# Performance work log

Hardware: AMD Instinct MI355X
Metric: run time of the kernel (lower is better)

Reference implementation:

```python
import jax, jax.numpy as jnp
import numpy as np

N_NODES = 50000

def _gcn_conv(x, W, b, src, dst, num_nodes):
    # PyG GCNConv: linear transform, then D^{-1/2} A_hat D^{-1/2} aggregation (A_hat has self-loops).
    xw = x @ W                                   # [N, out]
    ones = jnp.ones(src.shape[0], dtype=x.dtype)
    deg = jax.ops.segment_sum(ones, dst, num_segments=num_nodes)  # in-degree incl. self loop
    dinv = jnp.where(deg > 0, jax.lax.rsqrt(deg), 0.0)
    norm = dinv[src] * dinv[dst]                 # [E]
    msg = xw[src] * norm[:, None]                # [E, out] gather + scale
    out = jax.ops.segment_sum(msg, dst, num_segments=num_nodes)   # scatter-add
    return out + b

def _add_self_loops(edge_index, num_nodes):
    loop = jnp.arange(num_nodes, dtype=edge_index.dtype)
    src = jnp.concatenate([edge_index[0], loop])
    dst = jnp.concatenate([edge_index[1], loop])
    return src, dst

def setup_inputs() -> dict:
    key = jax.random.key(0)
    k = jax.random.split(key, 6)
    in_dim, hid_dim, out_dim = 256, 128, 64
    n_edges = 800000
    x = jax.random.normal(k[0], (N_NODES, in_dim), dtype=jnp.float32)
    edge_index = jax.random.randint(k[1], (2, n_edges), 0, N_NODES, dtype=jnp.int64)
    W1 = jax.random.normal(k[2], (in_dim, hid_dim), dtype=jnp.float32) / np.sqrt(in_dim)
    b1 = jnp.zeros((hid_dim,), dtype=jnp.float32)
    W2 = jax.random.normal(k[3], (hid_dim, out_dim), dtype=jnp.float32) / np.sqrt(hid_dim)
    b2 = jnp.zeros((out_dim,), dtype=jnp.float32)
    return {"x": x, "edge_index": edge_index, "W1": W1, "b1": b1, "W2": W2, "b2": b2}

def reference(x, edge_index, W1, b1, W2, b2):
    src, dst = _add_self_loops(edge_index, N_NODES)
    h = jnp.tanh(_gcn_conv(x, W1, b1, src, dst, N_NODES))
    out = _gcn_conv(h, W2, b2, src, dst, N_NODES)
    return out
```

## Files before the change

kernel.cpp:

```cpp
#include <hip/hip_runtime.h>

#define INDIM 256
#define HID 128
#define OUTD 64
#define BINSHIFT 8
#define MAXBIN 256

typedef _Float16 f16x8 __attribute__((ext_vector_type(8)));
typedef float    f32x4 __attribute__((ext_vector_type(4)));

__global__ __launch_bounds__(256) void k_setup(const float* __restrict__ W1, const float* __restrict__ W2,
                                               _Float16* __restrict__ W1t, _Float16* __restrict__ W2t,
                                               int* __restrict__ bin_counts) {
    constexpr int NW1 = HID * INDIM;
    constexpr int NW2 = OUTD * HID;
    int id = blockIdx.x * 256 + threadIdx.x;
    if (id < NW1) {
        int n = id / INDIM, k = id % INDIM;
        W1t[id] = (_Float16)W1[k * HID + n];
    } else if (id < NW1 + NW2) {
        int j = id - NW1;
        int n = j / HID, k = j % HID;
        W2t[j] = (_Float16)W2[k * OUTD + n];
    } else {
        int i = id - NW1 - NW2;
        if (i < MAXBIN) bin_counts[i] = 0;
    }
}

__global__ __launch_bounds__(256) void k_hist(const int* __restrict__ dst, int* __restrict__ bin_counts, int E) {
    __shared__ int h[MAXBIN];
    int tid = threadIdx.x;
    h[tid] = 0;
    __syncthreads();
    int base = blockIdx.x * 2048;
#pragma unroll
    for (int i = 0; i < 8; i++) {
        int e = base + i * 256 + tid;
        if (e < E) atomicAdd(&h[dst[e] >> BINSHIFT], 1);
    }
    __syncthreads();
    int v = h[tid];
    if (v) atomicAdd(&bin_counts[tid], v);
}

__global__ __launch_bounds__(256) void k_bscan(const int* __restrict__ bin_counts,
                                               int* __restrict__ bin_start, int* __restrict__ bin_cursor,
                                               int* __restrict__ row_start, int NBIN, int M, int E) {
    __shared__ int s[256];
    int tid = threadIdx.x;
    int v = (tid < NBIN) ? bin_counts[tid] : 0;
    s[tid] = v;
    __syncthreads();
#pragma unroll
    for (int off = 1; off < 256; off <<= 1) {
        int t = (tid >= off) ? s[tid - off] : 0;
        __syncthreads();
        s[tid] += t;
        __syncthreads();
    }
    if (tid < NBIN) {
        int excl = s[tid] - v;
        bin_start[tid] = excl;
        bin_cursor[tid] = excl;
    }
    if (tid == 0) {
        bin_start[NBIN] = E;
        row_start[M] = E;
    }
}

__global__ __launch_bounds__(256) void k_binfill(const int* __restrict__ src, const int* __restrict__ dst,
                                                 int* __restrict__ bin_cursor, int2* __restrict__ binned, int E) {
    __shared__ int h[MAXBIN];
    __shared__ int rb[MAXBIN];
    int tid = threadIdx.x;
    h[tid] = 0;
    __syncthreads();
    int base = blockIdx.x * 2048;
    int es[8], ed[8], rk[8];
#pragma unroll
    for (int i = 0; i < 8; i++) {
        int e = base + i * 256 + tid;
        if (e < E) {
            es[i] = src[e];
            ed[i] = dst[e];
            rk[i] = atomicAdd(&h[ed[i] >> BINSHIFT], 1);
        } else {
            ed[i] = -1;
        }
    }
    __syncthreads();
    int c = h[tid];
    if (c) rb[tid] = atomicAdd(&bin_cursor[tid], c);
    __syncthreads();
#pragma unroll
    for (int i = 0; i < 8; i++) {
        if (ed[i] >= 0) {
            binned[rb[ed[i] >> BINSHIFT] + rk[i]] = make_int2(es[i], ed[i]);
        }
    }
}

__global__ __launch_bounds__(256) void k_csr(const int2* __restrict__ binned, const int* __restrict__ bin_start,
                                             int* __restrict__ row_start, float* __restrict__ dinv,
                                             int* __restrict__ edge_src, int M) {
    __shared__ int cnt[256];
    __shared__ int s[256];
    __shared__ int cur[256];
    int b = blockIdx.x, tid = threadIdx.x;
    int beg = bin_start[b], end = bin_start[b + 1];
    cnt[tid] = 0;
    __syncthreads();
    for (int i = beg + tid; i < end; i += 256) {
        atomicAdd(&cnt[binned[i].y & 255], 1);
    }
    __syncthreads();
    int c = cnt[tid];
    s[tid] = c;
    __syncthreads();
#pragma unroll
    for (int off = 1; off < 256; off <<= 1) {
        int t = (tid >= off) ? s[tid - off] : 0;
        __syncthreads();
        s[tid] += t;
        __syncthreads();
    }
    int start = beg + s[tid] - c;
    int node = (b << BINSHIFT) + tid;
    if (node < M) {
        row_start[node] = start;
        dinv[node] = rsqrtf(1.0f + (float)c);
    }
    cur[tid] = start;
    __syncthreads();
    for (int i = beg + tid; i < end; i += 256) {
        int2 e = binned[i];
        int pos = atomicAdd(&cur[e.y & 255], 1);
        edge_src[pos] = e.x;
    }
}

template <int BN, int K, typename AT>
__global__ __launch_bounds__(256) void k_gemm_mfma(
    const AT* __restrict__ X, const _Float16* __restrict__ Wt,
    const float* __restrict__ dinv, _Float16* __restrict__ XW16, int M)
{
    constexpr int BM = 64;
    constexpr int BK = 32;
    constexpr int NT = BN / 16;
    constexpr int LDK = BK + 8;

    __shared__ __align__(16) _Float16 As[BM][LDK];
    __shared__ __align__(16) _Float16 Bs[BN][LDK];

    const int tid  = threadIdx.x;
    const int wave = tid >> 6;
    const int lane = tid & 63;
    const int m    = lane & 15;
    const int q    = lane >> 4;
    const int rb   = blockIdx.x * BM;

    f32x4 acc[NT];
#pragma unroll
    for (int t = 0; t < NT; t++) acc[t] = (f32x4){0.f, 0.f, 0.f, 0.f};

    for (int kt = 0; kt < K; kt += BK) {
        if (kt) __syncthreads();
        if constexpr (sizeof(AT) == 4) {
#pragma unroll
            for (int i = 0; i < BM * 8 / 256; i++) {
                int ch  = tid + i * 256;
                int row = ch >> 3;
                int c4  = ch & 7;
                int gr  = rb + row;
                float4 v = make_float4(0.f, 0.f, 0.f, 0.f);
                if (gr < M) v = *(const float4*)((const float*)X + (long)gr * K + kt + c4 * 4);
                _Float16* p = &As[row][c4 * 4];
                p[0] = (_Float16)v.x; p[1] = (_Float16)v.y;
                p[2] = (_Float16)v.z; p[3] = (_Float16)v.w;
            }
        } else {
            int row = tid >> 2;
            int c8  = tid & 3;
            int gr  = rb + row;
            uint4 v = make_uint4(0u, 0u, 0u, 0u);
            if (gr < M) v = *(const uint4*)((const _Float16*)X + (long)gr * K + kt + c8 * 8);
            *(uint4*)(&As[row][c8 * 8]) = v;
        }
#pragma unroll
        for (int i = 0; i < BN * 8 / 256; i++) {
            int ch = tid + i * 256;
            int n  = ch >> 3;
            int c4 = ch & 7;
            *(ushort4*)(&Bs[n][c4 * 4]) =
                *(const ushort4*)(Wt + (long)n * K + kt + c4 * 4);
        }
        __syncthreads();

        f16x8 af = *(const f16x8*)(&As[wave * 16 + m][q * 8]);
#pragma unroll
        for (int t = 0; t < NT; t++) {
            f16x8 bf = *(const f16x8*)(&Bs[t * 16 + m][q * 8]);
            acc[t] = __builtin_amdgcn_mfma_f32_16x16x32_f16(af, bf, acc[t], 0, 0, 0);
        }
    }

    int row0 = rb + wave * 16 + q * 4;
#pragma unroll
    for (int r = 0; r < 4; r++) {
        int row = row0 + r;
        if (row < M) {
            float di = dinv[row];
#pragma unroll
            for (int t = 0; t < NT; t++) {
                XW16[(long)row * BN + t * 16 + m] = (_Float16)(acc[t][r] * di);
            }
        }
    }
}

template <int F, bool TANH, typename OutT>
__global__ __launch_bounds__(256) void k_agg_csr(const int* __restrict__ row_start,
                                                 const int* __restrict__ edge_src,
                                                 const _Float16* __restrict__ feat,
                                                 const float* __restrict__ bias,
                                                 const float* __restrict__ dinv,
                                                 OutT* __restrict__ out, int M) {
    constexpr int LPN = F / 8;
    constexpr int NPB = 256 / LPN;
    int n = blockIdx.x * NPB + threadIdx.x / LPN;
    int c = threadIdx.x % LPN;
    if (n >= M) return;
    int beg = row_start[n], end = row_start[n + 1];

    f16x8 self = *(const f16x8*)(feat + (long)n * F + c * 8);
    float acc[8];
#pragma unroll
    for (int k = 0; k < 8; k++) acc[k] = (float)self[k];

    int j = beg;
    for (; j + 1 < end; j += 2) {
        int s0 = edge_src[j], s1 = edge_src[j + 1];
        f16x8 v0 = *(const f16x8*)(feat + (long)s0 * F + c * 8);
        f16x8 v1 = *(const f16x8*)(feat + (long)s1 * F + c * 8);
#pragma unroll
        for (int k = 0; k < 8; k++) acc[k] += (float)v0[k] + (float)v1[k];
    }
    if (j < end) {
        int s = edge_src[j];
        f16x8 v = *(const f16x8*)(feat + (long)s * F + c * 8);
#pragma unroll
        for (int k = 0; k < 8; k++) acc[k] += (float)v[k];
    }

    float di = dinv[n];
#pragma unroll
    for (int k = 0; k < 8; k++) acc[k] = bias[c * 8 + k] + di * acc[k];
    if (TANH) {
#pragma unroll
        for (int k = 0; k < 8; k++) acc[k] = tanhf(acc[k]);
    }
    if constexpr (sizeof(OutT) == 2) {
        f16x8 o;
#pragma unroll
        for (int k = 0; k < 8; k++) o[k] = (_Float16)acc[k];
        *(f16x8*)((_Float16*)out + (long)n * F + c * 8) = o;
    } else {
        float* p = (float*)out + (long)n * F + c * 8;
        *(float4*)(p)     = make_float4(acc[0], acc[1], acc[2], acc[3]);
        *(float4*)(p + 4) = make_float4(acc[4], acc[5], acc[6], acc[7]);
    }
}

extern "C" void kernel_launch(void* const* d_in, const int* in_sizes, int n_in,
                              void* d_out, int out_size, void* d_ws, size_t ws_size,
                              hipStream_t stream) {
    const float* x  = (const float*)d_in[0];
    const int*   ei = (const int*)d_in[1];
    const float* W1 = (const float*)d_in[2];
    const float* b1 = (const float*)d_in[3];
    const float* W2 = (const float*)d_in[4];
    const float* b2 = (const float*)d_in[5];
    float* out = (float*)d_out;

    const int M = in_sizes[0] / INDIM;
    const int E = in_sizes[1] / 2;
    const int* srcp = ei;
    const int* dstp = ei + E;

    const int Mp   = (M + 63) & ~63;
    const int NBIN = (M + 255) >> BINSHIFT;

    float*     dinv       = (float*)d_ws;
    int*       row_start  = (int*)(dinv + Mp);
    int*       bin_start  = row_start + Mp;
    int*       bin_cursor = bin_start + 258;
    int*       bin_counts = bin_cursor + MAXBIN;
    _Float16*  W1t        = (_Float16*)(bin_counts + MAXBIN);
    _Float16*  W2t        = W1t + HID * INDIM;
    int2*      binned     = (int2*)(W2t + OUTD * HID);
    int*       edge_src   = (int*)(binned + E);
    _Float16*  xw16       = (_Float16*)(edge_src + E);
    _Float16*  h16        = xw16 + (long)M * HID;
    _Float16*  hw16       = xw16;

    const int NWE = (E + 2047) / 2048;

    {
        int total = HID * INDIM + OUTD * HID + MAXBIN;
        k_setup<<<(total + 255) / 256, 256, 0, stream>>>(W1, W2, W1t, W2t, bin_counts);
    }
    k_hist<<<NWE, 256, 0, stream>>>(dstp, bin_counts, E);
    k_bscan<<<1, 256, 0, stream>>>(bin_counts, bin_start, bin_cursor, row_start, NBIN, M, E);
    k_binfill<<<NWE, 256, 0, stream>>>(srcp, dstp, bin_cursor, binned, E);
    k_csr<<<NBIN, 256, 0, stream>>>(binned, bin_start, row_start, dinv, edge_src, M);

    k_gemm_mfma<HID, INDIM, float><<<(M + 63) / 64, 256, 0, stream>>>(x, W1t, dinv, xw16, M);
    k_agg_csr<HID, true, _Float16><<<(M + 15) / 16, 256, 0, stream>>>(row_start, edge_src, xw16, b1, dinv, h16, M);

    k_gemm_mfma<OUTD, HID, _Float16><<<(M + 63) / 64, 256, 0, stream>>>(h16, W2t, dinv, hw16, M);
    k_agg_csr<OUTD, false, float><<<(M + 31) / 32, 256, 0, stream>>>(row_start, edge_src, hw16, b2, dinv, out, M);
}
```

Measured before the change: 230.8 us.

## Store features in 32-column chunk-major layout and aggregate per chunk

The GEMMs now write their fp16 outputs in a column-chunked layout of 32-wide slabs, and the aggregation runs as one launch per slab. Each gather pass then only touches a 3.2 MB feature slab that can stay resident in cache, which is meant to cut cache misses on random neighbor gathers. The per-edge loop is also unrolled by 4 to keep more loads in flight. The cost is extra kernel launches, re-reading the CSR indices once per chunk, and 64-byte gather granularity per node.

Result: slower. 248.8 us (+7.8%).

```diff
diff --git a/kernel.cpp b/kernel.cpp
--- a/kernel.cpp
+++ b/kernel.cpp
@@ -5,6 +5,7 @@
 #define OUTD 64
 #define BINSHIFT 8
 #define MAXBIN 256
+#define CW 32
 
 typedef _Float16 f16x8 __attribute__((ext_vector_type(8)));
 typedef float    f32x4 __attribute__((ext_vector_type(4)));
@@ -185,7 +186,8 @@
             int c8  = tid & 3;
             int gr  = rb + row;
             uint4 v = make_uint4(0u, 0u, 0u, 0u);
-            if (gr < M) v = *(const uint4*)((const _Float16*)X + (long)gr * K + kt + c8 * 8);
+            if (gr < M)
+                v = *(const uint4*)((const _Float16*)X + ((long)(kt / CW) * M + gr) * CW + c8 * 8);
             *(uint4*)(&As[row][c8 * 8]) = v;
         }
 #pragma unroll
@@ -214,49 +216,54 @@
             float di = dinv[row];
 #pragma unroll
             for (int t = 0; t < NT; t++) {
-                XW16[(long)row * BN + t * 16 + m] = (_Float16)(acc[t][r] * di);
+                int col = t * 16 + m;
+                XW16[((long)(col / CW) * M + row) * CW + (col & (CW - 1))] =
+                    (_Float16)(acc[t][r] * di);
             }
         }
     }
 }
 
-template <int F, bool TANH, typename OutT>
-__global__ __launch_bounds__(256) void k_agg_csr(const int* __restrict__ row_start,
-                                                 const int* __restrict__ edge_src,
-                                                 const _Float16* __restrict__ feat,
-                                                 const float* __restrict__ bias,
-                                                 const float* __restrict__ dinv,
-                                                 OutT* __restrict__ out, int M) {
-    constexpr int LPN = F / 8;
-    constexpr int NPB = 256 / LPN;
-    int n = blockIdx.x * NPB + threadIdx.x / LPN;
+template <bool TANH, typename OutT>
+__global__ __launch_bounds__(256) void k_agg_chunk(const int* __restrict__ row_start,
+                                                   const int* __restrict__ edge_src,
+                                                   const _Float16* __restrict__ featc,
+                                                   const float* __restrict__ biasc,
+                                                   const float* __restrict__ dinv,
+                                                   OutT* __restrict__ outc, int OS, int M) {
+    constexpr int LPN = CW / 8;
+    int n = blockIdx.x * (256 / LPN) + threadIdx.x / LPN;
     int c = threadIdx.x % LPN;
     if (n >= M) return;
     int beg = row_start[n], end = row_start[n + 1];
 
-    f16x8 self = *(const f16x8*)(feat + (long)n * F + c * 8);
+    f16x8 self = *(const f16x8*)(featc + (long)n * CW + c * 8);
     float acc[8];
 #pragma unroll
     for (int k = 0; k < 8; k++) acc[k] = (float)self[k];
 
     int j = beg;
-    for (; j + 1 < end; j += 2) {
+    for (; j + 3 < end; j += 4) {
         int s0 = edge_src[j], s1 = edge_src[j + 1];
-        f16x8 v0 = *(const f16x8*)(feat + (long)s0 * F + c * 8);
-        f16x8 v1 = *(const f16x8*)(feat + (long)s1 * F + c * 8);
-#pragma unroll
-        for (int k = 0; k < 8; k++) acc[k] += (float)v0[k] + (float)v1[k];
-    }
-    if (j < end) {
+        int s2 = edge_src[j + 2], s3 = edge_src[j + 3];
+        f16x8 v0 = *(const f16x8*)(featc + (long)s0 * CW + c * 8);
+        f16x8 v1 = *(const f16x8*)(featc + (long)s1 * CW + c * 8);
+        f16x8 v2 = *(const f16x8*)(featc + (long)s2 * CW + c * 8);
+        f16x8 v3 = *(const f16x8*)(featc + (long)s3 * CW + c * 8);
+#pragma unroll
+        for (int k = 0; k < 8; k++)
+            acc[k] += ((float)v0[k] + (float)v1[k]) + ((float)v2[k] + (float)v3[k]);
+    }
+    for (; j < end; j++) {
         int s = edge_src[j];
-        f16x8 v = *(const f16x8*)(feat + (long)s * F + c * 8);
+        f16x8 v = *(const f16x8*)(featc + (long)s * CW + c * 8);
 #pragma unroll
         for (int k = 0; k < 8; k++) acc[k] += (float)v[k];
     }
 
     float di = dinv[n];
 #pragma unroll
-    for (int k = 0; k < 8; k++) acc[k] = bias[c * 8 + k] + di * acc[k];
+    for (int k = 0; k < 8; k++) acc[k] = biasc[c * 8 + k] + di * acc[k];
     if (TANH) {
 #pragma unroll
         for (int k = 0; k < 8; k++) acc[k] = tanhf(acc[k]);
@@ -265,9 +272,9 @@
         f16x8 o;
 #pragma unroll
         for (int k = 0; k < 8; k++) o[k] = (_Float16)acc[k];
-        *(f16x8*)((_Float16*)out + (long)n * F + c * 8) = o;
+        *(f16x8*)((_Float16*)outc + (long)n * OS + c * 8) = o;
     } else {
-        float* p = (float*)out + (long)n * F + c * 8;
+        float* p = (float*)outc + (long)n * OS + c * 8;
         *(float4*)(p)     = make_float4(acc[0], acc[1], acc[2], acc[3]);
         *(float4*)(p + 4) = make_float4(acc[4], acc[5], acc[6], acc[7]);
     }
@@ -316,9 +323,21 @@
     k_binfill<<<NWE, 256, 0, stream>>>(srcp, dstp, bin_cursor, binned, E);
     k_csr<<<NBIN, 256, 0, stream>>>(binned, bin_start, row_start, dinv, edge_src, M);
 
+    const int GA = (M + 63) / 64;
+
     k_gemm_mfma<HID, INDIM, float><<<(M + 63) / 64, 256, 0, stream>>>(x, W1t, dinv, xw16, M);
-    k_agg_csr<HID, true, _Float16><<<(M + 15) / 16, 256, 0, stream>>>(row_start, edge_src, xw16, b1, dinv, h16, M);
+#pragma unroll
+    for (int ch = 0; ch < HID / CW; ch++) {
+        k_agg_chunk<true, _Float16><<<GA, 256, 0, stream>>>(
+            row_start, edge_src, xw16 + (long)ch * M * CW, b1 + ch * CW, dinv,
+            h16 + (long)ch * M * CW, CW, M);
+    }
 
     k_gemm_mfma<OUTD, HID, _Float16><<<(M + 63) / 64, 256, 0, stream>>>(h16, W2t, dinv, hw16, M);
-    k_agg_csr<OUTD, false, float><<<(M + 31) / 32, 256, 0, stream>>>(row_start, edge_src, hw16, b2, dinv, out, M);
-}
+#pragma unroll
+    for (int ch = 0; ch < OUTD / CW; ch++) {
+        k_agg_chunk<false, float><<<GA, 256, 0, stream>>>(
+            row_start, edge_src, hw16 + (long)ch * M * CW, b2 + ch * CW, dinv,
+            out + ch * CW, OUTD, M);
+    }
+}
```
